# Optimization experiments

Measured on AMD Instinct MI355X. Metric: run time of the kernel, lower is better.

## Reference

```python
import jax, jax.numpy as jnp
import numpy as np

HID = 1024
HEADS = 16
HEAD_DIM = HID // HEADS


def setup_inputs() -> dict:
    key = jax.random.key(0)
    ks = jax.random.split(key, 11)
    s = 1.0 / np.sqrt(HID)
    return {
        "query": jax.random.normal(ks[0], (4, 2048, HID), jnp.float32),
        "key": jax.random.normal(ks[1], (4, 2048, HID), jnp.float32),
        "value": jax.random.normal(ks[2], (4, 2048, HID), jnp.float32),
        "wq": jax.random.normal(ks[3], (HID, HID), jnp.float32) * s,
        "bq": jnp.zeros((HID,), jnp.float32),
        "wk": jax.random.normal(ks[4], (HID, HID), jnp.float32) * s,
        "bk": jnp.zeros((HID,), jnp.float32),
        "wv": jax.random.normal(ks[5], (HID, HID), jnp.float32) * s,
        "bv": jnp.zeros((HID,), jnp.float32),
        "wo": jax.random.normal(ks[6], (HID, HID), jnp.float32) * s,
        "bo": jnp.zeros((HID,), jnp.float32),
    }


def reference(query, key, value, wq, bq, wk, bk, wv, bv, wo, bo):
    b, s, _ = query.shape
    scale = jnp.sqrt(jnp.asarray(HEAD_DIM, query.dtype))
    # linear projections; weights stored as [in, out]
    Q = (query @ wq + bq).reshape(b, s, HEADS, HEAD_DIM).transpose(0, 2, 1, 3)
    K = (key @ wk + bk).reshape(b, s, HEADS, HEAD_DIM).transpose(0, 2, 1, 3)
    V = (value @ wv + bv).reshape(b, s, HEADS, HEAD_DIM).transpose(0, 2, 1, 3)
    energy = jnp.einsum('bhqd,bhkd->bhqk', Q, K) / scale  # [B,H,S,S]
    attention = jax.nn.softmax(energy, axis=-1)  # dropout p=0 -> identity
    x = jnp.einsum('bhqk,bhkd->bhqd', attention, V)
    x = x.transpose(0, 2, 1, 3).reshape(b, s, HID)
    return x @ wo + bo
```

## Files before the change

kernel.cpp:

```cpp
#include <hip/hip_runtime.h>
#include <hip/hip_bf16.h>

#define B_   4
#define S_   2048
#define HID_ 1024
#define H_   16
#define D_   64
#define M_   (B_ * S_)

typedef __attribute__((ext_vector_type(8)))  short bf16x8;
typedef __attribute__((ext_vector_type(4)))  float f32x4;
typedef __attribute__((ext_vector_type(16))) float f32x16;

#define GAS __attribute__((address_space(1)))
#define LAS __attribute__((address_space(3)))

__device__ __forceinline__ unsigned short f2bf(float f) {
    union { float f; unsigned int u; } x; x.f = f;
    unsigned int u = x.u;
    return (unsigned short)((u + 0x7fffu + ((u >> 16) & 1u)) >> 16);
}

__global__ __launch_bounds__(256)
void cast3(const float* __restrict__ q, const float* __restrict__ k, const float* __restrict__ v,
           unsigned short* __restrict__ oq, unsigned short* __restrict__ ok,
           unsigned short* __restrict__ ov) {
    const int sel = blockIdx.x >> 12;
    const int i = (blockIdx.x & 4095) * 256 + threadIdx.x;
    const float* in = (sel == 0) ? q : (sel == 1) ? k : v;
    unsigned short* out = (sel == 0) ? oq : (sel == 1) ? ok : ov;
    const f32x4 a = ((const f32x4*)in)[i * 2];
    const f32x4 b = ((const f32x4*)in)[i * 2 + 1];
    bf16x8 w;
#pragma unroll
    for (int j = 0; j < 4; j++) { w[j] = (short)f2bf(a[j]); w[4 + j] = (short)f2bf(b[j]); }
    ((bf16x8*)out)[i] = w;
}

__global__ void transpose_cast(const float* __restrict__ w0, const float* __restrict__ w1,
                               const float* __restrict__ w2, const float* __restrict__ w3,
                               unsigned short* __restrict__ o0, unsigned short* __restrict__ o1,
                               unsigned short* __restrict__ o2, unsigned short* __restrict__ o3) {
    __shared__ float t[32][33];
    const float* w = (blockIdx.z == 0) ? w0 : (blockIdx.z == 1) ? w1 : (blockIdx.z == 2) ? w2 : w3;
    unsigned short* o = (blockIdx.z == 0) ? o0 : (blockIdx.z == 1) ? o1 : (blockIdx.z == 2) ? o2 : o3;
    const int tx = threadIdx.x, ty = threadIdx.y;
    const int bx = blockIdx.x * 32, by = blockIdx.y * 32;
#pragma unroll
    for (int i = 0; i < 4; i++)
        t[ty + i * 8][tx] = w[(size_t)(by + ty + i * 8) * HID_ + bx + tx];
    __syncthreads();
#pragma unroll
    for (int i = 0; i < 4; i++)
        o[(size_t)(bx + ty + i * 8) * HID_ + by + tx] = f2bf(t[tx][ty + i * 8]);
}

__global__ __launch_bounds__(256)
void gemm_qkv(const unsigned short* __restrict__ aq, const unsigned short* __restrict__ ak,
              const unsigned short* __restrict__ av, const unsigned short* __restrict__ wqkvT,
              const float* __restrict__ bq, const float* __restrict__ bk,
              const float* __restrict__ bv, unsigned short* __restrict__ Qp,
              unsigned short* __restrict__ Kp, unsigned short* __restrict__ Vt, float cvt) {
    constexpr int BK = 32;
    __shared__ unsigned short smem[8704];
    unsigned short* As = smem;
    unsigned short* Bs = smem + 4096;

    const int tid  = threadIdx.x;
    const int lane = tid & 63;
    const int wave = tid >> 6;
    const int quad = lane >> 4;
    const int col  = lane & 15;
    const int wr   = (wave & 1) * 64;
    const int wc   = (wave >> 1) * 64;
    const int m0   = blockIdx.x * 128;
    const int third = blockIdx.y >> 3;
    const int n0l   = (blockIdx.y & 7) * 128;
    const bool vmode = (third == 2);

    const unsigned short* act = (third == 0) ? aq : (third == 1) ? ak : av;
    const float* bias = (third == 0) ? bq : (third == 1) ? bk : bv;
    unsigned short* outp = (third == 0) ? Qp : (third == 1) ? Kp : Vt;
    const float oscale = (third == 0) ? cvt : 1.f;

    const int grow = wave * 16 + (lane >> 2);
    const int gcol = (lane & 3) * 8;
    const unsigned short* wgp = wqkvT + (size_t)(third * HID_ + n0l + grow) * HID_ + gcol;
    const unsigned short* agp = act + (size_t)(m0 + grow) * HID_ + gcol;
    const unsigned short* rgp = vmode ? agp : wgp;
    const unsigned short* cgp = vmode ? wgp : agp;
    unsigned short* asb = &As[wave * 512];
    unsigned short* bsb = &Bs[wave * 512];

    f32x4 zero; zero[0] = 0.f; zero[1] = 0.f; zero[2] = 0.f; zero[3] = 0.f;
    f32x4 acc[4][4];
#pragma unroll
    for (int ri = 0; ri < 4; ri++)
#pragma unroll
        for (int ci = 0; ci < 4; ci++) acc[ri][ci] = zero;

    for (int kt = 0; kt < HID_; kt += BK) {
        __builtin_amdgcn_global_load_lds((const GAS unsigned int*)(rgp + kt),
                                         (LAS unsigned int*)asb, 16, 0, 0);
        __builtin_amdgcn_global_load_lds((const GAS unsigned int*)(rgp + kt + (size_t)64 * HID_),
                                         (LAS unsigned int*)(asb + 2048), 16, 0, 0);
        __builtin_amdgcn_global_load_lds((const GAS unsigned int*)(cgp + kt),
                                         (LAS unsigned int*)bsb, 16, 0, 0);
        __builtin_amdgcn_global_load_lds((const GAS unsigned int*)(cgp + kt + (size_t)64 * HID_),
                                         (LAS unsigned int*)(bsb + 2048), 16, 0, 0);
        __syncthreads();

        bf16x8 af[4], cf[4];
#pragma unroll
        for (int i = 0; i < 4; i++) af[i] = *(const bf16x8*)&As[(wr + i * 16 + col) * BK + quad * 8];
#pragma unroll
        for (int i = 0; i < 4; i++) cf[i] = *(const bf16x8*)&Bs[(wc + i * 16 + col) * BK + quad * 8];
#pragma unroll
        for (int ri = 0; ri < 4; ri++)
#pragma unroll
            for (int ci = 0; ci < 4; ci++)
                acc[ri][ci] = __builtin_amdgcn_mfma_f32_16x16x32_bf16(af[ri], cf[ci], acc[ri][ci], 0, 0, 0);
        __syncthreads();
    }

    unsigned short* RB = smem;
#pragma unroll
    for (int ph = 0; ph < 2; ph++) {
        if ((wave >> 1) == ph) {
#pragma unroll
            for (int ri = 0; ri < 4; ri++) {
                f32x4 bv4;
                if (!vmode) bv4 = *(const f32x4*)&bias[n0l + wr + ri * 16 + quad * 4];
#pragma unroll
                for (int ci = 0; ci < 4; ci++) {
                    float b0, b1, b2, b3;
                    if (!vmode) { b0 = bv4[0]; b1 = bv4[1]; b2 = bv4[2]; b3 = bv4[3]; }
                    else { b0 = b1 = b2 = b3 = bias[n0l + wc + ci * 16 + col]; }
                    const unsigned int u0 = f2bf((acc[ri][ci][0] + b0) * oscale);
                    const unsigned int u1 = f2bf((acc[ri][ci][1] + b1) * oscale);
                    const unsigned int u2 = f2bf((acc[ri][ci][2] + b2) * oscale);
                    const unsigned int u3 = f2bf((acc[ri][ci][3] + b3) * oscale);
                    uint2 w; w.x = u0 | (u1 << 16); w.y = u2 | (u3 << 16);
                    *(uint2*)&RB[(ci * 16 + col) * 136 + wr + ri * 16 + quad * 4] = w;
                }
            }
        }
        __syncthreads();
#pragma unroll
        for (int it = 0; it < 4; it++) {
            const int c   = it * 256 + tid;
            const int row = c >> 4, ch = c & 15;
            const bf16x8 v = *(const bf16x8*)&RB[row * 136 + ch * 8];
            if (!vmode) {
                const int n = n0l + ch * 8;
                const int h = n >> 6, d = n & 63;
                const int m = m0 + ph * 64 + row;
                *(bf16x8*)&outp[(((size_t)(m >> 11) * H_ + h) * S_ + (m & 2047)) * D_ + d] = v;
            } else {
                const int m = m0 + ch * 8;
                const int n = n0l + ph * 64 + row;
                const int h = n >> 6, d = n & 63;
                *(bf16x8*)&outp[(((size_t)(m >> 11) * H_ + h) * D_ + d) * S_ + (m & 2047)] = v;
            }
        }
        __syncthreads();
    }
}

__global__ __launch_bounds__(256)
void gemm_o(const unsigned short* __restrict__ A, const unsigned short* __restrict__ Bt,
            const float* __restrict__ bias, float* __restrict__ outp) {
    constexpr int BK = 32;
    __shared__ unsigned short As[128 * BK];
    __shared__ unsigned short Bs[128 * BK];

    const int tid  = threadIdx.x;
    const int lane = tid & 63;
    const int wave = tid >> 6;
    const int quad = lane >> 4;
    const int col  = lane & 15;
    const int wm   = (wave & 1) * 64;
    const int wn   = (wave >> 1) * 64;
    const int m0   = blockIdx.x * 128;
    const int n0   = blockIdx.y * 128;

    const int grow = wave * 16 + (lane >> 2);
    const int gcol = (lane & 3) * 8;
    const unsigned short* agp = A  + (size_t)(m0 + grow) * HID_ + gcol;
    const unsigned short* bgp = Bt + (size_t)(n0 + grow) * HID_ + gcol;
    unsigned short* asb = &As[wave * 512];
    unsigned short* bsb = &Bs[wave * 512];

    f32x4 zero; zero[0] = 0.f; zero[1] = 0.f; zero[2] = 0.f; zero[3] = 0.f;
    f32x4 acc[4][4];
#pragma unroll
    for (int mi = 0; mi < 4; mi++)
#pragma unroll
        for (int ni = 0; ni < 4; ni++) acc[mi][ni] = zero;

    for (int kt = 0; kt < HID_; kt += BK) {
        __builtin_amdgcn_global_load_lds((const GAS unsigned int*)(agp + kt),
                                         (LAS unsigned int*)asb, 16, 0, 0);
        __builtin_amdgcn_global_load_lds((const GAS unsigned int*)(agp + kt + (size_t)64 * HID_),
                                         (LAS unsigned int*)(asb + 2048), 16, 0, 0);
        __builtin_amdgcn_global_load_lds((const GAS unsigned int*)(bgp + kt),
                                         (LAS unsigned int*)bsb, 16, 0, 0);
        __builtin_amdgcn_global_load_lds((const GAS unsigned int*)(bgp + kt + (size_t)64 * HID_),
                                         (LAS unsigned int*)(bsb + 2048), 16, 0, 0);
        __syncthreads();

        bf16x8 af[4], bfr[4];
#pragma unroll
        for (int i = 0; i < 4; i++) af[i]  = *(const bf16x8*)&As[(wm + i * 16 + col) * BK + quad * 8];
#pragma unroll
        for (int i = 0; i < 4; i++) bfr[i] = *(const bf16x8*)&Bs[(wn + i * 16 + col) * BK + quad * 8];
#pragma unroll
        for (int mi = 0; mi < 4; mi++)
#pragma unroll
            for (int ni = 0; ni < 4; ni++)
                acc[mi][ni] = __builtin_amdgcn_mfma_f32_16x16x32_bf16(af[mi], bfr[ni], acc[mi][ni], 0, 0, 0);
        __syncthreads();
    }

#pragma unroll
    for (int ni = 0; ni < 4; ni++) {
        const int gn = n0 + wn + ni * 16 + col;
        const float bv = bias[gn];
#pragma unroll
        for (int mi = 0; mi < 4; mi++)
#pragma unroll
            for (int i = 0; i < 4; i++) {
                const int gm = m0 + wm + mi * 16 + quad * 4 + i;
                outp[(size_t)gm * HID_ + gn] = acc[mi][ni][i] + bv;
            }
    }
}

__global__ __launch_bounds__(256)
void attn_k(const unsigned short* __restrict__ Qp, const unsigned short* __restrict__ Kp,
            const unsigned short* __restrict__ Vt, unsigned short* __restrict__ Xc) {
    constexpr int LT = 72;
    __shared__ unsigned short Ks[64 * LT];
    __shared__ unsigned short Vs[64 * LT];
    __shared__ unsigned short Pb[4 * 32 * LT];

    const int tid  = threadIdx.x;
    const int lane = tid & 63;
    const int wave = tid >> 6;
    const int l31  = lane & 31;
    const int hw   = lane >> 5;
    const int bh   = blockIdx.y;
    const int q0   = blockIdx.x * 128 + wave * 32;

    const unsigned short* Qb = Qp + (size_t)bh * S_ * D_;
    const unsigned short* Kb = Kp + (size_t)bh * S_ * D_;
    const unsigned short* Vb = Vt + (size_t)bh * D_ * S_;

    bf16x8 qf[4];
#pragma unroll
    for (int ks = 0; ks < 4; ks++)
        qf[ks] = *(const bf16x8*)&Qb[(q0 + l31) * D_ + ks * 16 + hw * 8];

    f32x16 o[2];
#pragma unroll
    for (int t = 0; t < 2; t++)
#pragma unroll
        for (int i = 0; i < 16; i++) o[t][i] = 0.f;
    float lpart = 0.f;
    unsigned short* Pw = &Pb[wave * 32 * LT];

    for (int c0 = 0; c0 < S_; c0 += 64) {
#pragma unroll
        for (int it = 0; it < 2; it++) {
            const int c = it * 256 + tid;
            const int row = c >> 3, seg = (c & 7) * 8;
            *(bf16x8*)&Ks[row * LT + seg] = *(const bf16x8*)&Kb[(size_t)(c0 + row) * D_ + seg];
            *(bf16x8*)&Vs[row * LT + seg] = *(const bf16x8*)&Vb[(size_t)row * S_ + c0 + seg];
        }
        __syncthreads();

#pragma unroll
        for (int g = 0; g < 2; g++) {
            f32x16 e;
#pragma unroll
            for (int i = 0; i < 16; i++) e[i] = 0.f;
#pragma unroll
            for (int ks = 0; ks < 4; ks++) {
                const bf16x8 a = *(const bf16x8*)&Ks[(g * 32 + l31) * LT + ks * 16 + hw * 8];
                e = __builtin_amdgcn_mfma_f32_32x32x16_bf16(a, qf[ks], e, 0, 0, 0);
            }
#pragma unroll
            for (int grp = 0; grp < 4; grp++) {
                float p0 = __builtin_amdgcn_exp2f(e[grp * 4 + 0]);
                float p1 = __builtin_amdgcn_exp2f(e[grp * 4 + 1]);
                float p2 = __builtin_amdgcn_exp2f(e[grp * 4 + 2]);
                float p3 = __builtin_amdgcn_exp2f(e[grp * 4 + 3]);
                lpart += (p0 + p1) + (p2 + p3);
                const unsigned int u0 = __builtin_bit_cast(unsigned int, p0) + 0x8000u;
                const unsigned int u1 = __builtin_bit_cast(unsigned int, p1) + 0x8000u;
                const unsigned int u2 = __builtin_bit_cast(unsigned int, p2) + 0x8000u;
                const unsigned int u3 = __builtin_bit_cast(unsigned int, p3) + 0x8000u;
                uint2 w;
                w.x = __builtin_amdgcn_perm(u1, u0, 0x07060302u);
                w.y = __builtin_amdgcn_perm(u3, u2, 0x07060302u);
                *(uint2*)&Pw[l31 * LT + g * 32 + grp * 8 + hw * 4] = w;
            }
        }

#pragma unroll
        for (int ks = 0; ks < 4; ks++) {
            const bf16x8 pf = *(const bf16x8*)&Pw[l31 * LT + ks * 16 + hw * 8];
#pragma unroll
            for (int t = 0; t < 2; t++) {
                const bf16x8 vf = *(const bf16x8*)&Vs[(t * 32 + l31) * LT + ks * 16 + hw * 8];
                o[t] = __builtin_amdgcn_mfma_f32_32x32x16_bf16(vf, pf, o[t], 0, 0, 0);
            }
        }
        __syncthreads();
    }

    float l = lpart;
    l += __shfl_xor(l, 32);
    const float inv = 1.f / l;

    const int b = bh >> 4, h = bh & 15;
    const int s = q0 + l31;
    unsigned short* xp = &Xc[((size_t)(b * S_ + s)) * HID_ + h * D_];
#pragma unroll
    for (int t = 0; t < 2; t++)
#pragma unroll
        for (int grp = 0; grp < 4; grp++) {
            const unsigned int u0 = f2bf(o[t][grp * 4 + 0] * inv);
            const unsigned int u1 = f2bf(o[t][grp * 4 + 1] * inv);
            const unsigned int u2 = f2bf(o[t][grp * 4 + 2] * inv);
            const unsigned int u3 = f2bf(o[t][grp * 4 + 3] * inv);
            uint2 w; w.x = u0 | (u1 << 16); w.y = u2 | (u3 << 16);
            *(uint2*)&xp[t * 32 + grp * 8 + hw * 4] = w;
        }
}

extern "C" void kernel_launch(void* const* d_in, const int* in_sizes, int n_in,
                              void* d_out, int out_size, void* d_ws, size_t ws_size,
                              hipStream_t stream) {
    (void)in_sizes; (void)n_in; (void)out_size; (void)ws_size;
    const float* query = (const float*)d_in[0];
    const float* key   = (const float*)d_in[1];
    const float* value = (const float*)d_in[2];
    const float* wq    = (const float*)d_in[3];
    const float* bq    = (const float*)d_in[4];
    const float* wk    = (const float*)d_in[5];
    const float* bk    = (const float*)d_in[6];
    const float* wv    = (const float*)d_in[7];
    const float* bv    = (const float*)d_in[8];
    const float* wo    = (const float*)d_in[9];
    const float* bo    = (const float*)d_in[10];
    float* out = (float*)d_out;

    unsigned short* ws  = (unsigned short*)d_ws;
    const size_t WSZ = (size_t)HID_ * HID_;
    const size_t TSZ = (size_t)M_ * HID_;
    unsigned short* wqkvT = ws;
    unsigned short* woT = ws + 3 * WSZ;
    unsigned short* Qp  = woT + WSZ;
    unsigned short* Kp  = Qp + TSZ;
    unsigned short* Vt  = Kp + TSZ;
    unsigned short* Xc  = Vt + TSZ;
    unsigned short* Xb  = Xc + TSZ;

    const float cvt = 0.125f * 1.44269504f;

    transpose_cast<<<dim3(32, 32, 4), dim3(32, 8), 0, stream>>>(
        wq, wk, wv, wo, wqkvT, wqkvT + WSZ, wqkvT + 2 * WSZ, woT);

    cast3<<<3 * 4096, 256, 0, stream>>>(query, key, value, Xc, Xb, Xb + TSZ);

    gemm_qkv<<<dim3(M_ / 128, 24), 256, 0, stream>>>(
        Xc, Xb, Xb + TSZ, wqkvT, bq, bk, bv, Qp, Kp, Vt, cvt);

    attn_k<<<dim3(S_ / 128, B_ * H_), 256, 0, stream>>>(Qp, Kp, Vt, Xc);

    gemm_o<<<dim3(M_ / 128, HID_ / 128), 256, 0, stream>>>(Xc, woT, bo, out);
}
```

Baseline: 366.8 us.

## Process two N-tiles per block in projection GEMMs and stage gemm_o output via LDS

Both projection GEMMs now loop over two 128-wide N tiles inside each block, halving the grid. The aim is fewer blocks and some L2 reuse of the activation rows across the two tiles. gemm_o also swaps operand roles and writes its fp32 output through an LDS transpose buffer, so global stores become coalesced 16-byte row writes instead of scattered scalar stores. In exchange, each block's work is serialized, parallelism drops to 768 and 256 blocks, and gemm_o needs a larger LDS footprint.

```diff
diff --git a/kernel.cpp b/kernel.cpp
--- a/kernel.cpp
+++ b/kernel.cpp
@@ -74,8 +74,7 @@
     const int wr   = (wave & 1) * 64;
     const int wc   = (wave >> 1) * 64;
     const int m0   = blockIdx.x * 128;
-    const int third = blockIdx.y >> 3;
-    const int n0l   = (blockIdx.y & 7) * 128;
+    const int third = blockIdx.y >> 2;
     const bool vmode = (third == 2);
 
     const unsigned short* act = (third == 0) ? aq : (third == 1) ? ak : av;
@@ -85,85 +84,89 @@
 
     const int grow = wave * 16 + (lane >> 2);
     const int gcol = (lane & 3) * 8;
-    const unsigned short* wgp = wqkvT + (size_t)(third * HID_ + n0l + grow) * HID_ + gcol;
     const unsigned short* agp = act + (size_t)(m0 + grow) * HID_ + gcol;
-    const unsigned short* rgp = vmode ? agp : wgp;
-    const unsigned short* cgp = vmode ? wgp : agp;
     unsigned short* asb = &As[wave * 512];
     unsigned short* bsb = &Bs[wave * 512];
 
-    f32x4 zero; zero[0] = 0.f; zero[1] = 0.f; zero[2] = 0.f; zero[3] = 0.f;
-    f32x4 acc[4][4];
-#pragma unroll
-    for (int ri = 0; ri < 4; ri++)
-#pragma unroll
-        for (int ci = 0; ci < 4; ci++) acc[ri][ci] = zero;
-
-    for (int kt = 0; kt < HID_; kt += BK) {
-        __builtin_amdgcn_global_load_lds((const GAS unsigned int*)(rgp + kt),
-                                         (LAS unsigned int*)asb, 16, 0, 0);
-        __builtin_amdgcn_global_load_lds((const GAS unsigned int*)(rgp + kt + (size_t)64 * HID_),
-                                         (LAS unsigned int*)(asb + 2048), 16, 0, 0);
-        __builtin_amdgcn_global_load_lds((const GAS unsigned int*)(cgp + kt),
-                                         (LAS unsigned int*)bsb, 16, 0, 0);
-        __builtin_amdgcn_global_load_lds((const GAS unsigned int*)(cgp + kt + (size_t)64 * HID_),
-                                         (LAS unsigned int*)(bsb + 2048), 16, 0, 0);
-        __syncthreads();
-
-        bf16x8 af[4], cf[4];
-#pragma unroll
-        for (int i = 0; i < 4; i++) af[i] = *(const bf16x8*)&As[(wr + i * 16 + col) * BK + quad * 8];
-#pragma unroll
-        for (int i = 0; i < 4; i++) cf[i] = *(const bf16x8*)&Bs[(wc + i * 16 + col) * BK + quad * 8];
+    for (int nt = 0; nt < 2; nt++) {
+        const int n0l = (blockIdx.y & 3) * 256 + nt * 128;
+        const unsigned short* wgp = wqkvT + (size_t)(third * HID_ + n0l + grow) * HID_ + gcol;
+        const unsigned short* rgp = vmode ? agp : wgp;
+        const unsigned short* cgp = vmode ? wgp : agp;
+
+        f32x4 zero; zero[0] = 0.f; zero[1] = 0.f; zero[2] = 0.f; zero[3] = 0.f;
+        f32x4 acc[4][4];
 #pragma unroll
         for (int ri = 0; ri < 4; ri++)
 #pragma unroll
-            for (int ci = 0; ci < 4; ci++)
-                acc[ri][ci] = __builtin_amdgcn_mfma_f32_16x16x32_bf16(af[ri], cf[ci], acc[ri][ci], 0, 0, 0);
-        __syncthreads();
-    }
-
-    unsigned short* RB = smem;
-#pragma unroll
-    for (int ph = 0; ph < 2; ph++) {
-        if ((wave >> 1) == ph) {
-#pragma unroll
-            for (int ri = 0; ri < 4; ri++) {
-                f32x4 bv4;
-                if (!vmode) bv4 = *(const f32x4*)&bias[n0l + wr + ri * 16 + quad * 4];
-#pragma unroll
-                for (int ci = 0; ci < 4; ci++) {
-                    float b0, b1, b2, b3;
-                    if (!vmode) { b0 = bv4[0]; b1 = bv4[1]; b2 = bv4[2]; b3 = bv4[3]; }
-                    else { b0 = b1 = b2 = b3 = bias[n0l + wc + ci * 16 + col]; }
-                    const unsigned int u0 = f2bf((acc[ri][ci][0] + b0) * oscale);
-                    const unsigned int u1 = f2bf((acc[ri][ci][1] + b1) * oscale);
-                    const unsigned int u2 = f2bf((acc[ri][ci][2] + b2) * oscale);
-                    const unsigned int u3 = f2bf((acc[ri][ci][3] + b3) * oscale);
-                    uint2 w; w.x = u0 | (u1 << 16); w.y = u2 | (u3 << 16);
-                    *(uint2*)&RB[(ci * 16 + col) * 136 + wr + ri * 16 + quad * 4] = w;
+            for (int ci = 0; ci < 4; ci++) acc[ri][ci] = zero;
+
+        for (int kt = 0; kt < HID_; kt += BK) {
+            __builtin_amdgcn_global_load_lds((const GAS unsigned int*)(rgp + kt),
+                                             (LAS unsigned int*)asb, 16, 0, 0);
+            __builtin_amdgcn_global_load_lds((const GAS unsigned int*)(rgp + kt + (size_t)64 * HID_),
+                                             (LAS unsigned int*)(asb + 2048), 16, 0, 0);
+            __builtin_amdgcn_global_load_lds((const GAS unsigned int*)(cgp + kt),
+                                             (LAS unsigned int*)bsb, 16, 0, 0);
+            __builtin_amdgcn_global_load_lds((const GAS unsigned int*)(cgp + kt + (size_t)64 * HID_),
+                                             (LAS unsigned int*)(bsb + 2048), 16, 0, 0);
+            __syncthreads();
+
+            bf16x8 af[4], cf[4];
+#pragma unroll
+            for (int i = 0; i < 4; i++) af[i] = *(const bf16x8*)&As[(wr + i * 16 + col) * BK + quad * 8];
+#pragma unroll
+            for (int i = 0; i < 4; i++) cf[i] = *(const bf16x8*)&Bs[(wc + i * 16 + col) * BK + quad * 8];
+#pragma unroll
+            for (int ri = 0; ri < 4; ri++)
+#pragma unroll
+                for (int ci = 0; ci < 4; ci++)
+                    acc[ri][ci] = __builtin_amdgcn_mfma_f32_16x16x32_bf16(af[ri], cf[ci], acc[ri][ci], 0, 0, 0);
+            __syncthreads();
+        }
+
+        unsigned short* RB = smem;
+#pragma unroll
+        for (int ph = 0; ph < 2; ph++) {
+            if ((wave >> 1) == ph) {
+#pragma unroll
+                for (int ri = 0; ri < 4; ri++) {
+                    f32x4 bv4;
+                    if (!vmode) bv4 = *(const f32x4*)&bias[n0l + wr + ri * 16 + quad * 4];
+#pragma unroll
+                    for (int ci = 0; ci < 4; ci++) {
+                        float b0, b1, b2, b3;
+                        if (!vmode) { b0 = bv4[0]; b1 = bv4[1]; b2 = bv4[2]; b3 = bv4[3]; }
+                        else { b0 = b1 = b2 = b3 = bias[n0l + wc + ci * 16 + col]; }
+                        const unsigned int u0 = f2bf((acc[ri][ci][0] + b0) * oscale);
+                        const unsigned int u1 = f2bf((acc[ri][ci][1] + b1) * oscale);
+                        const unsigned int u2 = f2bf((acc[ri][ci][2] + b2) * oscale);
+                        const unsigned int u3 = f2bf((acc[ri][ci][3] + b3) * oscale);
+                        uint2 w; w.x = u0 | (u1 << 16); w.y = u2 | (u3 << 16);
+                        *(uint2*)&RB[(ci * 16 + col) * 136 + wr + ri * 16 + quad * 4] = w;
+                    }
                 }
             }
-        }
-        __syncthreads();
-#pragma unroll
-        for (int it = 0; it < 4; it++) {
-            const int c   = it * 256 + tid;
-            const int row = c >> 4, ch = c & 15;
-            const bf16x8 v = *(const bf16x8*)&RB[row * 136 + ch * 8];
-            if (!vmode) {
-                const int n = n0l + ch * 8;
-                const int h = n >> 6, d = n & 63;
-                const int m = m0 + ph * 64 + row;
-                *(bf16x8*)&outp[(((size_t)(m >> 11) * H_ + h) * S_ + (m & 2047)) * D_ + d] = v;
-            } else {
-                const int m = m0 + ch * 8;
-                const int n = n0l + ph * 64 + row;
-                const int h = n >> 6, d = n & 63;
-                *(bf16x8*)&outp[(((size_t)(m >> 11) * H_ + h) * D_ + d) * S_ + (m & 2047)] = v;
-            }
-        }
-        __syncthreads();
+            __syncthreads();
+#pragma unroll
+            for (int it = 0; it < 4; it++) {
+                const int c   = it * 256 + tid;
+                const int row = c >> 4, ch = c & 15;
+                const bf16x8 v = *(const bf16x8*)&RB[row * 136 + ch * 8];
+                if (!vmode) {
+                    const int n = n0l + ch * 8;
+                    const int h = n >> 6, d = n & 63;
+                    const int m = m0 + ph * 64 + row;
+                    *(bf16x8*)&outp[(((size_t)(m >> 11) * H_ + h) * S_ + (m & 2047)) * D_ + d] = v;
+                } else {
+                    const int m = m0 + ch * 8;
+                    const int n = n0l + ph * 64 + row;
+                    const int h = n >> 6, d = n & 63;
+                    *(bf16x8*)&outp[(((size_t)(m >> 11) * H_ + h) * D_ + d) * S_ + (m & 2047)] = v;
+                }
+            }
+            __syncthreads();
+        }
     }
 }
 
@@ -171,68 +174,85 @@
 void gemm_o(const unsigned short* __restrict__ A, const unsigned short* __restrict__ Bt,
             const float* __restrict__ bias, float* __restrict__ outp) {
     constexpr int BK = 32;
-    __shared__ unsigned short As[128 * BK];
-    __shared__ unsigned short Bs[128 * BK];
+    __shared__ float smemf[64 * 132];
+    unsigned short* As = (unsigned short*)smemf;
+    unsigned short* Bs = As + 4096;
 
     const int tid  = threadIdx.x;
     const int lane = tid & 63;
     const int wave = tid >> 6;
     const int quad = lane >> 4;
     const int col  = lane & 15;
+    const int wn   = (wave >> 1) * 64;
     const int wm   = (wave & 1) * 64;
-    const int wn   = (wave >> 1) * 64;
     const int m0   = blockIdx.x * 128;
-    const int n0   = blockIdx.y * 128;
 
     const int grow = wave * 16 + (lane >> 2);
     const int gcol = (lane & 3) * 8;
-    const unsigned short* agp = A  + (size_t)(m0 + grow) * HID_ + gcol;
-    const unsigned short* bgp = Bt + (size_t)(n0 + grow) * HID_ + gcol;
+    const unsigned short* agp = A + (size_t)(m0 + grow) * HID_ + gcol;
     unsigned short* asb = &As[wave * 512];
     unsigned short* bsb = &Bs[wave * 512];
 
-    f32x4 zero; zero[0] = 0.f; zero[1] = 0.f; zero[2] = 0.f; zero[3] = 0.f;
-    f32x4 acc[4][4];
-#pragma unroll
-    for (int mi = 0; mi < 4; mi++)
-#pragma unroll
-        for (int ni = 0; ni < 4; ni++) acc[mi][ni] = zero;
-
-    for (int kt = 0; kt < HID_; kt += BK) {
-        __builtin_amdgcn_global_load_lds((const GAS unsigned int*)(agp + kt),
-                                         (LAS unsigned int*)asb, 16, 0, 0);
-        __builtin_amdgcn_global_load_lds((const GAS unsigned int*)(agp + kt + (size_t)64 * HID_),
-                                         (LAS unsigned int*)(asb + 2048), 16, 0, 0);
-        __builtin_amdgcn_global_load_lds((const GAS unsigned int*)(bgp + kt),
-                                         (LAS unsigned int*)bsb, 16, 0, 0);
-        __builtin_amdgcn_global_load_lds((const GAS unsigned int*)(bgp + kt + (size_t)64 * HID_),
-                                         (LAS unsigned int*)(bsb + 2048), 16, 0, 0);
-        __syncthreads();
-
-        bf16x8 af[4], bfr[4];
-#pragma unroll
-        for (int i = 0; i < 4; i++) af[i]  = *(const bf16x8*)&As[(wm + i * 16 + col) * BK + quad * 8];
-#pragma unroll
-        for (int i = 0; i < 4; i++) bfr[i] = *(const bf16x8*)&Bs[(wn + i * 16 + col) * BK + quad * 8];
-#pragma unroll
-        for (int mi = 0; mi < 4; mi++)
-#pragma unroll
-            for (int ni = 0; ni < 4; ni++)
-                acc[mi][ni] = __builtin_amdgcn_mfma_f32_16x16x32_bf16(af[mi], bfr[ni], acc[mi][ni], 0, 0, 0);
-        __syncthreads();
-    }
-
-#pragma unroll
-    for (int ni = 0; ni < 4; ni++) {
-        const int gn = n0 + wn + ni * 16 + col;
-        const float bv = bias[gn];
-#pragma unroll
-        for (int mi = 0; mi < 4; mi++)
-#pragma unroll
-            for (int i = 0; i < 4; i++) {
-                const int gm = m0 + wm + mi * 16 + quad * 4 + i;
-                outp[(size_t)gm * HID_ + gn] = acc[mi][ni][i] + bv;
-            }
+    for (int nt = 0; nt < 2; nt++) {
+        const int n0l = blockIdx.y * 256 + nt * 128;
+        const unsigned short* wgp = Bt + (size_t)(n0l + grow) * HID_ + gcol;
+
+        f32x4 zero; zero[0] = 0.f; zero[1] = 0.f; zero[2] = 0.f; zero[3] = 0.f;
+        f32x4 acc[4][4];
+#pragma unroll
+        for (int ri = 0; ri < 4; ri++)
+#pragma unroll
+            for (int ci = 0; ci < 4; ci++) acc[ri][ci] = zero;
+
+        for (int kt = 0; kt < HID_; kt += BK) {
+            __builtin_amdgcn_global_load_lds((const GAS unsigned int*)(wgp + kt),
+                                             (LAS unsigned int*)asb, 16, 0, 0);
+            __builtin_amdgcn_global_load_lds((const GAS unsigned int*)(wgp + kt + (size_t)64 * HID_),
+                                             (LAS unsigned int*)(asb + 2048), 16, 0, 0);
+            __builtin_amdgcn_global_load_lds((const GAS unsigned int*)(agp + kt),
+                                             (LAS unsigned int*)bsb, 16, 0, 0);
+            __builtin_amdgcn_global_load_lds((const GAS unsigned int*)(agp + kt + (size_t)64 * HID_),
+                                             (LAS unsigned int*)(bsb + 2048), 16, 0, 0);
+            __syncthreads();
+
+            bf16x8 wf[4], af[4];
+#pragma unroll
+            for (int i = 0; i < 4; i++) wf[i] = *(const bf16x8*)&As[(wn + i * 16 + col) * BK + quad * 8];
+#pragma unroll
+            for (int i = 0; i < 4; i++) af[i] = *(const bf16x8*)&Bs[(wm + i * 16 + col) * BK + quad * 8];
+#pragma unroll
+            for (int ri = 0; ri < 4; ri++)
+#pragma unroll
+                for (int ci = 0; ci < 4; ci++)
+                    acc[ri][ci] = __builtin_amdgcn_mfma_f32_16x16x32_bf16(wf[ri], af[ci], acc[ri][ci], 0, 0, 0);
+            __syncthreads();
+        }
+
+#pragma unroll
+        for (int ph = 0; ph < 2; ph++) {
+            if ((wave & 1) == ph) {
+#pragma unroll
+                for (int ri = 0; ri < 4; ri++) {
+                    const f32x4 bv4 = *(const f32x4*)&bias[n0l + wn + ri * 16 + quad * 4];
+#pragma unroll
+                    for (int ci = 0; ci < 4; ci++) {
+                        f32x4 v;
+#pragma unroll
+                        for (int i = 0; i < 4; i++) v[i] = acc[ri][ci][i] + bv4[i];
+                        *(f32x4*)&smemf[(ci * 16 + col) * 132 + wn + ri * 16 + quad * 4] = v;
+                    }
+                }
+            }
+            __syncthreads();
+#pragma unroll
+            for (int it = 0; it < 8; it++) {
+                const int c   = it * 256 + tid;
+                const int row = c >> 5, ch = c & 31;
+                const f32x4 v = *(const f32x4*)&smemf[row * 132 + ch * 4];
+                *(f32x4*)&outp[(size_t)(m0 + ph * 64 + row) * HID_ + n0l + ch * 4] = v;
+            }
+            __syncthreads();
+        }
     }
 }
 
@@ -374,10 +394,10 @@
 
     cast3<<<3 * 4096, 256, 0, stream>>>(query, key, value, Xc, Xb, Xb + TSZ);
 
-    gemm_qkv<<<dim3(M_ / 128, 24), 256, 0, stream>>>(
+    gemm_qkv<<<dim3(M_ / 128, 12), 256, 0, stream>>>(
         Xc, Xb, Xb + TSZ, wqkvT, bq, bk, bv, Qp, Kp, Vt, cvt);
 
     attn_k<<<dim3(S_ / 128, B_ * H_), 256, 0, stream>>>(Qp, Kp, Vt, Xc);
 
-    gemm_o<<<dim3(M_ / 128, HID_ / 128), 256, 0, stream>>>(Xc, woT, bo, out);
-}
+    gemm_o<<<dim3(M_ / 128, 4), 256, 0, stream>>>(Xc, woT, bo, out);
+}
```

Result: slower. 459.8 us (+25.4%).
